# Kernel optimization log

Hardware: AMD Instinct MI355X
Metric: run time of the kernel (lower is better)

## Reference

```python
import jax, jax.numpy as jnp
import numpy as np
import math


def get_alibi_slopes(n_heads: int) -> np.ndarray:
    # Bloom-style ALiBi slopes.
    cp2 = 2 ** math.floor(math.log2(n_heads))
    base = 2.0 ** (-(2.0 ** -(math.log2(cp2) - 3)))
    slopes = base ** np.arange(1, cp2 + 1, dtype=np.float32)
    if cp2 != n_heads:
        extra_base = 2.0 ** (-(2.0 ** -(math.log2(2 * cp2) - 3)))
        extra = extra_base ** np.arange(1, 2 * (n_heads - cp2) + 1, 2, dtype=np.float32)
        slopes = np.concatenate([slopes, extra])
    return slopes.astype(np.float32)


def setup_inputs() -> dict:
    key = jax.random.key(0)
    k1, k2, k3 = jax.random.split(key, 3)
    B, S, D, H = 2, 2048, 2048, 16
    T = B * S
    return {
        "hidden_states": jax.random.normal(k1, (T, D), dtype=jnp.float32) * 0.02,
        "qkv_weight": jax.random.normal(k2, (3, D, D), dtype=jnp.float32) * 0.02,
        "o_proj_weight": jax.random.normal(k3, (D, D), dtype=jnp.float32) * 0.02,
        "batch": B,
        "seq_len": S,
        "n_heads": H,
    }


def reference(hidden_states, qkv_weight, o_proj_weight, batch, seq_len, n_heads):
    T, D = hidden_states.shape
    head_dim = D // n_heads
    sm_scale = 1.0 / math.sqrt(head_dim)
    slopes = jnp.asarray(get_alibi_slopes(n_heads))  # [H]

    # QKV projection: equivalent of bmm(hidden.expand(3,-1,-1), qkv_weight)
    qkv = jnp.einsum("td,cde->cte", hidden_states, qkv_weight)  # [3, T, D]
    q, k, v = qkv.reshape(3, batch, seq_len, n_heads, head_dim)

    # Varlen causal attention with ALiBi (prefill / context phase).
    scores = jnp.einsum("bqhd,bkhd->bhqk", q, k) * sm_scale  # [B,H,S,S]
    pos = jnp.arange(seq_len)
    rel = (pos[None, :] - pos[:, None]).astype(jnp.float32)  # k_idx - q_idx
    scores = scores + slopes[None, :, None, None] * rel[None, None]
    causal = pos[None, :] <= pos[:, None]  # [S,S]
    scores = jnp.where(causal[None, None], scores, jnp.finfo(scores.dtype).min)
    probs = jax.nn.softmax(scores, axis=-1)
    attn = jnp.einsum("bhqk,bkhd->bqhd", probs, v)  # [B,S,H,Dh]

    attn = attn.reshape(T, D)
    return attn @ o_proj_weight
```

## Files before the change

### kernel.cpp

```cpp
#include <hip/hip_runtime.h>
#include <math.h>
#include <stdint.h>

typedef __bf16 bf16x8_t __attribute__((ext_vector_type(8)));
typedef float  f32x4_t  __attribute__((ext_vector_type(4)));
typedef unsigned short u16;


__device__ __forceinline__ u16 f2bf(float f) {
  unsigned u = __float_as_uint(f);
  u += 0x7FFFu + ((u >> 16) & 1u);
  return (u16)(u >> 16);
}

__device__ __forceinline__ u16 bf16bits(float f) {
  __bf16 b = (__bf16)f;
  return __builtin_bit_cast(u16, b);
}

__device__ __forceinline__ void gload_lds16(const u16* gsrc, u16* ldst) {
  __builtin_amdgcn_global_load_lds(
      (__attribute__((address_space(1))) void*)(const_cast<u16*>(gsrc)),
      (__attribute__((address_space(3))) void*)(ldst),
      16, 0, 0);
}

__device__ __forceinline__ int sw8(int row, int e) { return e ^ ((row & 7) << 3); }

__device__ __forceinline__ void store_out(float* C, long idx, float v) { C[idx] = v; }
__device__ __forceinline__ void store_out(u16* C, long idx, float v) { C[idx] = f2bf(v); }

__device__ __forceinline__ float alibi_slope(int h, int H) {
  int cp2 = 1, lg = 0;
  while (cp2 * 2 <= H) { cp2 *= 2; lg++; }
  if (h < cp2) {
    double e = exp2((double)-(lg - 3));
    return (float)exp2(-e * (double)(h + 1));
  } else {
    double e = exp2((double)-(lg + 1 - 3));
    return (float)exp2(-e * (double)(2 * (h - cp2) + 1));
  }
}

#define FENCE() asm volatile("" ::: "memory")
#define BARRIER() do { FENCE(); __builtin_amdgcn_s_barrier(); \
                       __builtin_amdgcn_sched_barrier(0); FENCE(); } while (0)
#define WAITLGKM() do { asm volatile("s_waitcnt lgkmcnt(0)" ::: "memory"); \
                        __builtin_amdgcn_sched_barrier(0); } while (0)


__global__ __launch_bounds__(256) void k_cast_bf16(const float* __restrict__ in,
                                                   u16* __restrict__ out, long n) {
  long i = ((long)blockIdx.x * 256 + threadIdx.x) * 4;
  if (i + 3 < n) {
    float4 v = *reinterpret_cast<const float4*>(in + i);
    ushort4 o;
    o.x = f2bf(v.x); o.y = f2bf(v.y); o.z = f2bf(v.z); o.w = f2bf(v.w);
    *reinterpret_cast<ushort4*>(out + i) = o;
  }
}


__global__ __launch_bounds__(256) void k_transpose_cast4(const float* __restrict__ in0,
                                                         const float* __restrict__ in1,
                                                         u16* __restrict__ out,
                                                         int R, int C) {
  __shared__ float tile[32][33];
  const float* inz = (blockIdx.z < 3) ? (in0 + (long)blockIdx.z * R * C) : in1;
  u16* outz = out + (long)blockIdx.z * R * C;
  const int tx = threadIdx.x & 31, ty = threadIdx.x >> 5;
  const int r0 = blockIdx.y * 32, c0 = blockIdx.x * 32;
#pragma unroll
  for (int i = 0; i < 4; ++i)
    tile[ty + i * 8][tx] = inz[(long)(r0 + ty + i * 8) * C + c0 + tx];
  __syncthreads();
#pragma unroll
  for (int i = 0; i < 4; ++i)
    outz[(long)(c0 + ty + i * 8) * R + r0 + tx] = f2bf(tile[tx][ty + i * 8]);
}


__device__ __forceinline__ void stage16(const u16* __restrict__ g, long grow0, int K,
                                        int kt, int lr0, u16 (*lds)[64], int lane) {
  const int e = (lane & 7) * 8;
#pragma unroll
  for (int i = 0; i < 2; ++i) {
    const int r = lr0 + i * 8 + (lane >> 3);
    gload_lds16(g + (grow0 + r) * (long)K + kt + (e ^ ((r & 7) << 3)), &lds[lr0 + i * 8][0]);
  }
}

__device__ __forceinline__ void stage8(const u16* __restrict__ g, long grow0, int K,
                                       int kt, int lr0, u16 (*lds)[64], int lane) {
  const int e = (lane & 7) * 8;
  const int r = lr0 + (lane >> 3);
  gload_lds16(g + (grow0 + r) * (long)K + kt + (e ^ ((r & 7) << 3)), &lds[lr0][0]);
}


template <typename OUT_T>
__global__ __launch_bounds__(512, 2) void k_gemm8(const u16* __restrict__ A,
                                                  const u16* __restrict__ Bt,
                                                  OUT_T* __restrict__ Cb,
                                                  int M, int N, int K, long matStride,
                                                  float qs, u16* __restrict__ Vt) {
  __shared__ u16 As[2][256][64];
  __shared__ u16 Bs[2][256][64];

  const int tid = threadIdx.x, wid = tid >> 6, lane = tid & 63;
  const int wr = wid >> 2, wc = wid & 3;
  const int frow = lane & 15, fk8 = (lane >> 4) * 8;
  const int orow = (lane >> 4) * 4, ocol = lane & 15;

  const int nwg = gridDim.x * gridDim.y;
  const int orig = blockIdx.y * gridDim.x + blockIdx.x;
  const int q = nwg >> 3, rr = nwg & 7;
  const int xcd = orig & 7, sl = orig >> 3;
  const int wg = (xcd < rr ? xcd * (q + 1) : rr * (q + 1) + (xcd - rr) * q) + sl;
  const int by = wg / gridDim.x, bx = wg % gridDim.x;

  const long abase = (long)by * 256, bbase = (long)bx * 256;

  const int bg0 = (wid >> 1) * 64 + (wid & 1) * 16;
  const int ag0 = (wid >> 2) * 128 + (wid & 3) * 16;

  f32x4_t acc[8][4];
#pragma unroll
  for (int m = 0; m < 8; ++m)
#pragma unroll
    for (int n = 0; n < 4; ++n)
#pragma unroll
      for (int r = 0; r < 4; ++r) acc[m][n][r] = 0.f;

  const int nt = K >> 6;

  stage16(A, abase, K, 0, ag0, As[0], lane);
  stage16(Bt, bbase, K, 0, bg0, Bs[0], lane);
  stage16(Bt, bbase, K, 0, bg0 + 32, Bs[0], lane);
  stage16(A, abase, K, 0, ag0 + 64, As[0], lane);
  asm volatile("s_waitcnt vmcnt(4)" ::: "memory");
  BARRIER();

  bf16x8_t afr[4][2], bfr[4][2];
  int cur = 0;

  for (int t = 0; t < nt; ++t) {
    const int ktn = (t + 1) << 6;
    const bool hn = (t + 1 < nt);
    const int nb = cur ^ 1;

#pragma unroll
    for (int m = 0; m < 4; ++m) {
      const int r = wr * 128 + m * 16 + frow;
      afr[m][0] = *reinterpret_cast<const bf16x8_t*>(&As[cur][r][sw8(r, fk8)]);
      afr[m][1] = *reinterpret_cast<const bf16x8_t*>(&As[cur][r][sw8(r, 32 + fk8)]);
    }
#pragma unroll
    for (int n = 0; n < 2; ++n) {
      const int r = wc * 64 + n * 16 + frow;
      bfr[n][0] = *reinterpret_cast<const bf16x8_t*>(&Bs[cur][r][sw8(r, fk8)]);
      bfr[n][1] = *reinterpret_cast<const bf16x8_t*>(&Bs[cur][r][sw8(r, 32 + fk8)]);
    }
    if (hn) stage16(A, abase, K, ktn, ag0, As[nb], lane);
    BARRIER();
    WAITLGKM();
    __builtin_amdgcn_s_setprio(1);
#pragma unroll
    for (int m = 0; m < 4; ++m)
#pragma unroll
      for (int n = 0; n < 2; ++n) {
        acc[m][n] = __builtin_amdgcn_mfma_f32_16x16x32_bf16(afr[m][0], bfr[n][0], acc[m][n], 0, 0, 0);
        acc[m][n] = __builtin_amdgcn_mfma_f32_16x16x32_bf16(afr[m][1], bfr[n][1], acc[m][n], 0, 0, 0);
      }
    __builtin_amdgcn_s_setprio(0);
    if (hn) asm volatile("s_waitcnt vmcnt(4)" ::: "memory");
    else    asm volatile("s_waitcnt vmcnt(2)" ::: "memory");
    BARRIER();

#pragma unroll
    for (int n = 0; n < 2; ++n) {
      const int r = wc * 64 + 32 + n * 16 + frow;
      bfr[2 + n][0] = *reinterpret_cast<const bf16x8_t*>(&Bs[cur][r][sw8(r, fk8)]);
      bfr[2 + n][1] = *reinterpret_cast<const bf16x8_t*>(&Bs[cur][r][sw8(r, 32 + fk8)]);
    }
    if (hn) stage16(Bt, bbase, K, ktn, bg0, Bs[nb], lane);
    BARRIER();
    WAITLGKM();
    __builtin_amdgcn_s_setprio(1);
#pragma unroll
    for (int m = 0; m < 4; ++m)
#pragma unroll
      for (int n = 0; n < 2; ++n) {
        acc[m][2 + n] = __builtin_amdgcn_mfma_f32_16x16x32_bf16(afr[m][0], bfr[2 + n][0], acc[m][2 + n], 0, 0, 0);
        acc[m][2 + n] = __builtin_amdgcn_mfma_f32_16x16x32_bf16(afr[m][1], bfr[2 + n][1], acc[m][2 + n], 0, 0, 0);
      }
    __builtin_amdgcn_s_setprio(0);
    if (!hn) asm volatile("s_waitcnt vmcnt(0)" ::: "memory");
    BARRIER();

#pragma unroll
    for (int m = 0; m < 4; ++m) {
      const int r = wr * 128 + 64 + m * 16 + frow;
      afr[m][0] = *reinterpret_cast<const bf16x8_t*>(&As[cur][r][sw8(r, fk8)]);
      afr[m][1] = *reinterpret_cast<const bf16x8_t*>(&As[cur][r][sw8(r, 32 + fk8)]);
    }
    if (hn) stage16(Bt, bbase, K, ktn, bg0 + 32, Bs[nb], lane);
    BARRIER();
    WAITLGKM();
    __builtin_amdgcn_s_setprio(1);
#pragma unroll
    for (int m = 0; m < 4; ++m)
#pragma unroll
      for (int n = 0; n < 2; ++n) {
        acc[4 + m][n] = __builtin_amdgcn_mfma_f32_16x16x32_bf16(afr[m][0], bfr[n][0], acc[4 + m][n], 0, 0, 0);
        acc[4 + m][n] = __builtin_amdgcn_mfma_f32_16x16x32_bf16(afr[m][1], bfr[n][1], acc[4 + m][n], 0, 0, 0);
      }
    __builtin_amdgcn_s_setprio(0);
    BARRIER();

    if (hn) stage16(A, abase, K, ktn, ag0 + 64, As[nb], lane);
    __builtin_amdgcn_s_setprio(1);
#pragma unroll
    for (int m = 0; m < 4; ++m)
#pragma unroll
      for (int n = 0; n < 2; ++n) {
        acc[4 + m][2 + n] = __builtin_amdgcn_mfma_f32_16x16x32_bf16(afr[m][0], bfr[2 + n][0], acc[4 + m][2 + n], 0, 0, 0);
        acc[4 + m][2 + n] = __builtin_amdgcn_mfma_f32_16x16x32_bf16(afr[m][1], bfr[2 + n][1], acc[4 + m][2 + n], 0, 0, 0);
      }
    __builtin_amdgcn_s_setprio(0);
    if (hn) asm volatile("s_waitcnt vmcnt(4)" ::: "memory");
    BARRIER();

    cur ^= 1;
  }

  const int mat = (int)(bbase >> 11);
  if (Vt != nullptr && mat == 2) {
#pragma unroll
    for (int m = 0; m < 8; ++m)
#pragma unroll
      for (int n = 0; n < 4; ++n)
#pragma unroll
        for (int r = 0; r < 4; ++r) {
          const long row = abase + wr * 128 + m * 16 + orow + r;
          const int col = (int)bbase + wc * 64 + n * 16 + ocol;
          const int e = col & 2047, hh = e >> 7, dd = e & 127;
          const long bb = row >> 11, ss = row & 2047;
          Vt[(((bb << 4) + hh) * 128 + dd) * 2048 + ss] = bf16bits(acc[m][n][r]);
        }
  } else {
#pragma unroll
    for (int m = 0; m < 8; ++m)
#pragma unroll
      for (int n = 0; n < 4; ++n)
#pragma unroll
        for (int r = 0; r < 4; ++r) {
          const long row = abase + wr * 128 + m * 16 + orow + r;
          const int col = (int)bbase + wc * 64 + n * 16 + ocol;
          const float sc = (mat == 0) ? qs : 1.0f;
          const long idx = (long)mat * matStride + row * 2048 + (col & 2047);
          store_out(Cb, idx, acc[m][n][r] * sc);
        }
  }
}


template <typename OUT_T>
__global__ __launch_bounds__(512, 2) void k_gemm2(const u16* __restrict__ A,
                                                  const u16* __restrict__ Bt,
                                                  OUT_T* __restrict__ Cb,
                                                  int M, int N, int K, long matStride,
                                                  float qs) {
  __shared__ u16 As[2][128][64];
  __shared__ u16 Bs[2][256][64];

  const int tid = threadIdx.x, wid = tid >> 6, lane = tid & 63;
  const int wr = wid >> 2, wc = wid & 3;
  const int frow = lane & 15, fk8 = (lane >> 4) * 8;
  const int orow = (lane >> 4) * 4, ocol = lane & 15;

  const int nwg = gridDim.x * gridDim.y;
  const int orig = blockIdx.y * gridDim.x + blockIdx.x;
  const int q = nwg >> 3, rr = nwg & 7;
  const int xcd = orig & 7, sl = orig >> 3;
  const int wg = (xcd < rr ? xcd * (q + 1) : rr * (q + 1) + (xcd - rr) * q) + sl;
  const int by = wg / gridDim.x, bx = wg % gridDim.x;

  const long abase = (long)by * 128, bbase = (long)bx * 256;

  const int bg0 = (wid >> 1) * 64 + (wid & 1) * 16;
  const int ag0 = ((wid & 1) << 6) + ((wid >> 1) << 3);

  f32x4_t acc[4][4];
#pragma unroll
  for (int m = 0; m < 4; ++m)
#pragma unroll
    for (int n = 0; n < 4; ++n)
#pragma unroll
      for (int r = 0; r < 4; ++r) acc[m][n][r] = 0.f;

  const int nt = K >> 6;

  stage16(Bt, bbase, K, 0, bg0, Bs[0], lane);
  stage16(Bt, bbase, K, 0, bg0 + 32, Bs[0], lane);
  stage8 (A,  abase, K, 0, ag0, As[0], lane);
  stage8 (A,  abase, K, 0, ag0 + 32, As[0], lane);
  asm volatile("s_waitcnt vmcnt(1)" ::: "memory");
  BARRIER();

  bf16x8_t bfr[4][2], afr[2][2];
  int cur = 0;

  for (int t = 0; t < nt; ++t) {
    const int ktn = (t + 1) << 6;
    const bool hn = (t + 1 < nt);
    const int nb = cur ^ 1;

#pragma unroll
    for (int n = 0; n < 4; ++n) {
      const int r = wc * 64 + n * 16 + frow;
      bfr[n][0] = *reinterpret_cast<const bf16x8_t*>(&Bs[cur][r][sw8(r, fk8)]);
      bfr[n][1] = *reinterpret_cast<const bf16x8_t*>(&Bs[cur][r][sw8(r, 32 + fk8)]);
    }
#pragma unroll
    for (int m = 0; m < 2; ++m) {
      const int r = wr * 64 + m * 16 + frow;
      afr[m][0] = *reinterpret_cast<const bf16x8_t*>(&As[cur][r][sw8(r, fk8)]);
      afr[m][1] = *reinterpret_cast<const bf16x8_t*>(&As[cur][r][sw8(r, 32 + fk8)]);
    }
    if (hn) {
      stage16(Bt, bbase, K, ktn, bg0, Bs[nb], lane);
      stage16(Bt, bbase, K, ktn, bg0 + 32, Bs[nb], lane);
    }
    BARRIER();
    WAITLGKM();
    __builtin_amdgcn_s_setprio(1);
#pragma unroll
    for (int m = 0; m < 2; ++m)
#pragma unroll
      for (int n = 0; n < 4; ++n) {
        acc[m][n] = __builtin_amdgcn_mfma_f32_16x16x32_bf16(afr[m][0], bfr[n][0], acc[m][n], 0, 0, 0);
        acc[m][n] = __builtin_amdgcn_mfma_f32_16x16x32_bf16(afr[m][1], bfr[n][1], acc[m][n], 0, 0, 0);
      }
    __builtin_amdgcn_s_setprio(0);
    if (hn) asm volatile("s_waitcnt vmcnt(4)" ::: "memory");
    else    asm volatile("s_waitcnt vmcnt(0)" ::: "memory");
    BARRIER();

#pragma unroll
    for (int m = 0; m < 2; ++m) {
      const int r = wr * 64 + 32 + m * 16 + frow;
      afr[m][0] = *reinterpret_cast<const bf16x8_t*>(&As[cur][r][sw8(r, fk8)]);
      afr[m][1] = *reinterpret_cast<const bf16x8_t*>(&As[cur][r][sw8(r, 32 + fk8)]);
    }
    if (hn) {
      stage8(A, abase, K, ktn, ag0, As[nb], lane);
      stage8(A, abase, K, ktn, ag0 + 32, As[nb], lane);
    }
    BARRIER();
    WAITLGKM();
    __builtin_amdgcn_s_setprio(1);
#pragma unroll
    for (int m = 0; m < 2; ++m)
#pragma unroll
      for (int n = 0; n < 4; ++n) {
        acc[2 + m][n] = __builtin_amdgcn_mfma_f32_16x16x32_bf16(afr[m][0], bfr[n][0], acc[2 + m][n], 0, 0, 0);
        acc[2 + m][n] = __builtin_amdgcn_mfma_f32_16x16x32_bf16(afr[m][1], bfr[n][1], acc[2 + m][n], 0, 0, 0);
      }
    __builtin_amdgcn_s_setprio(0);
    if (hn) asm volatile("s_waitcnt vmcnt(1)" ::: "memory");
    BARRIER();

    cur ^= 1;
  }

#pragma unroll
  for (int m = 0; m < 4; ++m)
#pragma unroll
    for (int n = 0; n < 4; ++n)
#pragma unroll
      for (int r = 0; r < 4; ++r) {
        const long row = abase + wr * 64 + m * 16 + orow + r;
        const int col = (int)bbase + wc * 64 + n * 16 + ocol;
        const float sc = ((col >> 11) == 0) ? qs : 1.0f;
        const long idx = (long)(col >> 11) * matStride + row * 2048 + (col & 2047);
        store_out(Cb, idx, acc[m][n][r] * sc);
      }
}


__global__ __launch_bounds__(256) void k_attn(const u16* __restrict__ Q,
                                              const u16* __restrict__ Kb,
                                              const u16* __restrict__ Vt,
                                              u16* __restrict__ Out,
                                              int B, int S, int H, int D,
                                              float log2e) {
  __shared__ u16 Ks[2][64][128];
  __shared__ u16 Vs[2][128][64];
  __shared__ u16 Ps[64][64];

  const int tid = threadIdx.x, wid = tid >> 6, lane = tid & 63;

  const int nq = gridDim.x, nbh = gridDim.y;
  const int lin = blockIdx.x + nq * blockIdx.y;
  const int qb0 = lin / nbh;
  const int bh  = lin % nbh;
  const int qb  = (qb0 < nq / 2) ? qb0 : (nq + nq / 2 - 1 - qb0);

  const int b = bh / H, h = bh % H;
  const int Dh = D / H;

  const float slope2 = alibi_slope(h, H) * log2e;
  const long qrow0 = (long)b * S + qb * 64 + wid * 16;

  const int frow = lane & 15;
  const int fk8  = (lane >> 4) * 8;
  const int orow = (lane >> 4) * 4;
  const int ocol = lane & 15;

  bf16x8_t aq[4];
#pragma unroll
  for (int kk = 0; kk < 4; ++kk)
    aq[kk] = *reinterpret_cast<const bf16x8_t*>(
        Q + (qrow0 + frow) * (long)D + h * Dh + kk * 32 + fk8);

  float cw[4];
#pragma unroll
  for (int n = 0; n < 4; ++n) cw[n] = slope2 * (float)(n * 16 + ocol);

  f32x4_t oacc[8];
#pragma unroll
  for (int no = 0; no < 8; ++no)
#pragma unroll
    for (int r = 0; r < 4; ++r) oacc[no][r] = 0.f;

  float Mrun[4], lrun[4];
#pragma unroll
  for (int r = 0; r < 4; ++r) { Mrun[r] = -3.0e38f; lrun[r] = 0.f; }

  const u16* kbase = Kb + (long)b * S * D + h * Dh;
  const u16* vbase = Vt + (long)bh * Dh * S;

  auto STAGE = [&](int kt, int bi) {
#pragma unroll
    for (int i = 0; i < 4; ++i) {
      const int lr = i * 16 + wid * 4;
      const int r  = lr + (lane >> 4);
      gload_lds16(kbase + ((long)kt * 64 + r) * (long)D + sw8(r, (lane & 15) * 8),
                  &Ks[bi][lr][0]);
    }
#pragma unroll
    for (int i = 0; i < 4; ++i) {
      const int lr = i * 32 + wid * 8;
      const int r  = lr + (lane >> 3);
      gload_lds16(vbase + (long)r * S + kt * 64 + sw8(r, (lane & 7) * 8),
                  &Vs[bi][lr][0]);
    }
  };

  STAGE(qb, 0);
  asm volatile("s_waitcnt vmcnt(0)" ::: "memory");
  BARRIER();

  int cur = 0;

  for (int kt = qb; kt >= 0; --kt) {
    if (kt > 0) STAGE(kt - 1, cur ^ 1);

    f32x4_t sacc[4];
#pragma unroll
    for (int n = 0; n < 4; ++n)
#pragma unroll
      for (int r = 0; r < 4; ++r) sacc[n][r] = 0.f;

    __builtin_amdgcn_s_setprio(1);
#pragma unroll
    for (int kk = 0; kk < 4; ++kk) {
      bf16x8_t bk[4];
#pragma unroll
      for (int n = 0; n < 4; ++n) {
        const int krow = n * 16 + frow;
        bk[n] = *reinterpret_cast<const bf16x8_t*>(&Ks[cur][krow][sw8(krow, kk * 32 + fk8)]);
      }
#pragma unroll
      for (int n = 0; n < 4; ++n)
        sacc[n] = __builtin_amdgcn_mfma_f32_16x16x32_bf16(aq[kk], bk[n], sacc[n], 0, 0, 0);
    }
    __builtin_amdgcn_s_setprio(0);

    const float tb = slope2 * (float)(kt << 6);
    float cbn[4];
#pragma unroll
    for (int n = 0; n < 4; ++n) cbn[n] = tb + cw[n];

    float tmax[4];
#pragma unroll
    for (int r = 0; r < 4; ++r) tmax[r] = -3.0e38f;

    if (kt == qb) {
#pragma unroll
      for (int n = 0; n < 4; ++n)
#pragma unroll
        for (int r = 0; r < 4; ++r) {
          float v = sacc[n][r] + cbn[n];
          v = (n * 16 + ocol <= wid * 16 + orow + r) ? v : -1.0e30f;
          sacc[n][r] = v;
          tmax[r] = fmaxf(tmax[r], v);
        }
    } else {
#pragma unroll
      for (int n = 0; n < 4; ++n)
#pragma unroll
        for (int r = 0; r < 4; ++r) {
          const float v = sacc[n][r] + cbn[n];
          sacc[n][r] = v;
          tmax[r] = fmaxf(tmax[r], v);
        }
    }
#pragma unroll
    for (int r = 0; r < 4; ++r) {
      float t = tmax[r];
      t = fmaxf(t, __shfl_xor(t, 1));
      t = fmaxf(t, __shfl_xor(t, 2));
      t = fmaxf(t, __shfl_xor(t, 4));
      t = fmaxf(t, __shfl_xor(t, 8));
      tmax[r] = t;
    }

    int need = 0;
#pragma unroll
    for (int r = 0; r < 4; ++r) need |= (tmax[r] > Mrun[r] + 11.0f) ? 1 : 0;
    if (__any(need)) {
#pragma unroll
      for (int r = 0; r < 4; ++r) {
        const float mnew = fmaxf(Mrun[r], tmax[r]);
        const float alpha = exp2f(Mrun[r] - mnew);
        Mrun[r] = mnew;
        lrun[r] *= alpha;
#pragma unroll
        for (int no = 0; no < 8; ++no) oacc[no][r] *= alpha;
      }
    }

    float tsum[4];
#pragma unroll
    for (int r = 0; r < 4; ++r) tsum[r] = 0.f;
#pragma unroll
    for (int n = 0; n < 4; ++n)
#pragma unroll
      for (int r = 0; r < 4; ++r) {
        const float p = exp2f(sacc[n][r] - Mrun[r]);
        tsum[r] += p;
        const int prow = wid * 16 + orow + r;
        Ps[prow][sw8(prow, n * 16 + ocol)] = bf16bits(p);
      }
#pragma unroll
    for (int r = 0; r < 4; ++r) {
      float t = tsum[r];
      t += __shfl_xor(t, 1);
      t += __shfl_xor(t, 2);
      t += __shfl_xor(t, 4);
      t += __shfl_xor(t, 8);
      lrun[r] += t;
    }

    WAITLGKM();
    BARRIER();

    __builtin_amdgcn_s_setprio(1);
#pragma unroll
    for (int kk = 0; kk < 2; ++kk) {
      const int prow = wid * 16 + frow;
      bf16x8_t pa = *reinterpret_cast<const bf16x8_t*>(&Ps[prow][sw8(prow, kk * 32 + fk8)]);
#pragma unroll
      for (int no = 0; no < 8; ++no) {
        const int vrow = no * 16 + frow;
        bf16x8_t bv = *reinterpret_cast<const bf16x8_t*>(&Vs[cur][vrow][sw8(vrow, kk * 32 + fk8)]);
        oacc[no] = __builtin_amdgcn_mfma_f32_16x16x32_bf16(pa, bv, oacc[no], 0, 0, 0);
      }
    }
    __builtin_amdgcn_s_setprio(0);

    if (kt > 0) {
      asm volatile("s_waitcnt vmcnt(0)" ::: "memory");
      BARRIER();
      cur ^= 1;
    }
  }

#pragma unroll
  for (int r = 0; r < 4; ++r) {
    const float rl = 1.0f / lrun[r];
    const long trow = qrow0 + orow + r;
#pragma unroll
    for (int no = 0; no < 8; ++no)
      Out[trow * (long)D + h * Dh + no * 16 + ocol] = bf16bits(oacc[no][r] * rl);
  }
}


extern "C" void kernel_launch(void* const* d_in, const int* in_sizes, int n_in,
                              void* d_out, int out_size, void* d_ws, size_t ws_size,
                              hipStream_t stream) {
  const float* hs   = (const float*)d_in[0];
  const float* qkvw = (const float*)d_in[1];
  const float* ow   = (const float*)d_in[2];

  const int D = 2048, B = 2, H = 16;
  const long TD = (long)in_sizes[0];
  const long DD = (long)in_sizes[2];
  const int T = (int)(TD / D);
  const int S = T / B;
  const int Dh = D / H;
  const float log2e = 1.44269504f;
  const float qs = (1.0f / sqrtf((float)Dh)) * log2e;

  u16* ws  = (u16*)d_ws;
  u16* hsb = ws;
  u16* wt  = ws + TD;
  u16* owt = wt + 3 * DD;
  u16* qkv = owt + DD;
  u16* vt   = qkv + 2 * TD;
  u16* attn = hsb;

  k_cast_bf16<<<dim3((unsigned)(TD / 1024)), 256, 0, stream>>>(hs, hsb, TD);
  k_transpose_cast4<<<dim3(D / 32, D / 32, 4), 256, 0, stream>>>(qkvw, ow, wt, D, D);
  k_gemm8<u16><<<dim3((3 * D) / 256, T / 256), 512, 0, stream>>>(
      hsb, wt, qkv, T, 3 * D, D, TD, qs, vt);
  k_attn<<<dim3(S / 64, B * H), 256, 0, stream>>>(
      qkv, qkv + TD, vt, attn, B, S, H, D, log2e);
  k_gemm2<float><<<dim3(D / 256, T / 128), 512, 0, stream>>>(
      attn, owt, (float*)d_out, T, D, D, 0L, 1.0f);
}
```

Before: 283.4 us.

## Enlarge attention query tile to 128 rows with two M-subtiles per wave

Each attention block now handles 128 query rows instead of 64, and each wave computes two 16-row subtiles against the same K and V tiles in shared memory. This halves the number of K/V tile loads per query row and doubles the MFMA work per LDS read of K/V. Waves whose rows lie entirely before the current key tile skip compute but still join the barriers. In exchange the grid is halved, register pressure rises from the doubled accumulators, and causal work is less balanced across waves.

```diff
diff --git a/kernel.cpp b/kernel.cpp
--- a/kernel.cpp
+++ b/kernel.cpp
@@ -397,7 +397,7 @@
                                               float log2e) {
   __shared__ u16 Ks[2][64][128];
   __shared__ u16 Vs[2][128][64];
-  __shared__ u16 Ps[64][64];
+  __shared__ u16 Ps[128][64];
 
   const int tid = threadIdx.x, wid = tid >> 6, lane = tid & 63;
 
@@ -411,32 +411,39 @@
   const int Dh = D / H;
 
   const float slope2 = alibi_slope(h, H) * log2e;
-  const long qrow0 = (long)b * S + qb * 64 + wid * 16;
+  const long qrow0 = (long)b * S + qb * 128 + wid * 32;
+  const int qg0 = qb * 128 + wid * 32;
 
   const int frow = lane & 15;
   const int fk8  = (lane >> 4) * 8;
   const int orow = (lane >> 4) * 4;
   const int ocol = lane & 15;
 
-  bf16x8_t aq[4];
-#pragma unroll
-  for (int kk = 0; kk < 4; ++kk)
-    aq[kk] = *reinterpret_cast<const bf16x8_t*>(
-        Q + (qrow0 + frow) * (long)D + h * Dh + kk * 32 + fk8);
+  bf16x8_t aq[2][4];
+#pragma unroll
+  for (int m = 0; m < 2; ++m)
+#pragma unroll
+    for (int kk = 0; kk < 4; ++kk)
+      aq[m][kk] = *reinterpret_cast<const bf16x8_t*>(
+          Q + (qrow0 + m * 16 + frow) * (long)D + h * Dh + kk * 32 + fk8);
 
   float cw[4];
 #pragma unroll
   for (int n = 0; n < 4; ++n) cw[n] = slope2 * (float)(n * 16 + ocol);
 
-  f32x4_t oacc[8];
-#pragma unroll
-  for (int no = 0; no < 8; ++no)
-#pragma unroll
-    for (int r = 0; r < 4; ++r) oacc[no][r] = 0.f;
-
-  float Mrun[4], lrun[4];
-#pragma unroll
-  for (int r = 0; r < 4; ++r) { Mrun[r] = -3.0e38f; lrun[r] = 0.f; }
+  f32x4_t oacc[2][8];
+#pragma unroll
+  for (int m = 0; m < 2; ++m)
+#pragma unroll
+    for (int no = 0; no < 8; ++no)
+#pragma unroll
+      for (int r = 0; r < 4; ++r) oacc[m][no][r] = 0.f;
+
+  float Mrun[2][4], lrun[2][4];
+#pragma unroll
+  for (int m = 0; m < 2; ++m)
+#pragma unroll
+    for (int r = 0; r < 4; ++r) { Mrun[m][r] = -3.0e38f; lrun[m][r] = 0.f; }
 
   const u16* kbase = Kb + (long)b * S * D + h * Dh;
   const u16* vbase = Vt + (long)bh * Dh * S;
@@ -458,128 +465,162 @@
     }
   };
 
-  STAGE(qb, 0);
+  STAGE(2 * qb + 1, 0);
   asm volatile("s_waitcnt vmcnt(0)" ::: "memory");
   BARRIER();
 
   int cur = 0;
 
-  for (int kt = qb; kt >= 0; --kt) {
+  for (int kt = 2 * qb + 1; kt >= 0; --kt) {
     if (kt > 0) STAGE(kt - 1, cur ^ 1);
 
-    f32x4_t sacc[4];
-#pragma unroll
-    for (int n = 0; n < 4; ++n)
-#pragma unroll
-      for (int r = 0; r < 4; ++r) sacc[n][r] = 0.f;
-
-    __builtin_amdgcn_s_setprio(1);
-#pragma unroll
-    for (int kk = 0; kk < 4; ++kk) {
-      bf16x8_t bk[4];
-#pragma unroll
-      for (int n = 0; n < 4; ++n) {
-        const int krow = n * 16 + frow;
-        bk[n] = *reinterpret_cast<const bf16x8_t*>(&Ks[cur][krow][sw8(krow, kk * 32 + fk8)]);
-      }
-#pragma unroll
-      for (int n = 0; n < 4; ++n)
-        sacc[n] = __builtin_amdgcn_mfma_f32_16x16x32_bf16(aq[kk], bk[n], sacc[n], 0, 0, 0);
-    }
-    __builtin_amdgcn_s_setprio(0);
-
-    const float tb = slope2 * (float)(kt << 6);
-    float cbn[4];
-#pragma unroll
-    for (int n = 0; n < 4; ++n) cbn[n] = tb + cw[n];
-
-    float tmax[4];
-#pragma unroll
-    for (int r = 0; r < 4; ++r) tmax[r] = -3.0e38f;
-
-    if (kt == qb) {
-#pragma unroll
-      for (int n = 0; n < 4; ++n)
+    const bool active = (kt * 64) <= (qg0 + 31);
+
+    if (active) {
+      f32x4_t sacc[2][4];
+#pragma unroll
+      for (int m = 0; m < 2; ++m)
+#pragma unroll
+        for (int n = 0; n < 4; ++n)
+#pragma unroll
+          for (int r = 0; r < 4; ++r) sacc[m][n][r] = 0.f;
+
+      __builtin_amdgcn_s_setprio(1);
+#pragma unroll
+      for (int kk = 0; kk < 4; ++kk) {
+        bf16x8_t bk[4];
+#pragma unroll
+        for (int n = 0; n < 4; ++n) {
+          const int krow = n * 16 + frow;
+          bk[n] = *reinterpret_cast<const bf16x8_t*>(&Ks[cur][krow][sw8(krow, kk * 32 + fk8)]);
+        }
+#pragma unroll
+        for (int m = 0; m < 2; ++m)
+#pragma unroll
+          for (int n = 0; n < 4; ++n)
+            sacc[m][n] = __builtin_amdgcn_mfma_f32_16x16x32_bf16(aq[m][kk], bk[n], sacc[m][n], 0, 0, 0);
+      }
+      __builtin_amdgcn_s_setprio(0);
+
+      const float tb = slope2 * (float)(kt << 6);
+      float cbn[4];
+#pragma unroll
+      for (int n = 0; n < 4; ++n) cbn[n] = tb + cw[n];
+
+      float tmax[2][4];
+#pragma unroll
+      for (int m = 0; m < 2; ++m)
+#pragma unroll
+        for (int r = 0; r < 4; ++r) tmax[m][r] = -3.0e38f;
+
+      if (kt >= 2 * qb) {
+#pragma unroll
+        for (int m = 0; m < 2; ++m)
+#pragma unroll
+          for (int n = 0; n < 4; ++n)
+#pragma unroll
+            for (int r = 0; r < 4; ++r) {
+              const int kg = (kt << 6) + n * 16 + ocol;
+              const int qg = qg0 + m * 16 + orow + r;
+              float v = sacc[m][n][r] + cbn[n];
+              v = (kg <= qg) ? v : -1.0e30f;
+              sacc[m][n][r] = v;
+              tmax[m][r] = fmaxf(tmax[m][r], v);
+            }
+      } else {
+#pragma unroll
+        for (int m = 0; m < 2; ++m)
+#pragma unroll
+          for (int n = 0; n < 4; ++n)
+#pragma unroll
+            for (int r = 0; r < 4; ++r) {
+              const float v = sacc[m][n][r] + cbn[n];
+              sacc[m][n][r] = v;
+              tmax[m][r] = fmaxf(tmax[m][r], v);
+            }
+      }
+#pragma unroll
+      for (int m = 0; m < 2; ++m)
 #pragma unroll
         for (int r = 0; r < 4; ++r) {
-          float v = sacc[n][r] + cbn[n];
-          v = (n * 16 + ocol <= wid * 16 + orow + r) ? v : -1.0e30f;
-          sacc[n][r] = v;
-          tmax[r] = fmaxf(tmax[r], v);
+          float t = tmax[m][r];
+          t = fmaxf(t, __shfl_xor(t, 1));
+          t = fmaxf(t, __shfl_xor(t, 2));
+          t = fmaxf(t, __shfl_xor(t, 4));
+          t = fmaxf(t, __shfl_xor(t, 8));
+          tmax[m][r] = t;
         }
-    } else {
-#pragma unroll
-      for (int n = 0; n < 4; ++n)
+
+      int need = 0;
+#pragma unroll
+      for (int m = 0; m < 2; ++m)
+#pragma unroll
+        for (int r = 0; r < 4; ++r) need |= (tmax[m][r] > Mrun[m][r] + 11.0f) ? 1 : 0;
+      if (__any(need)) {
+#pragma unroll
+        for (int m = 0; m < 2; ++m)
+#pragma unroll
+          for (int r = 0; r < 4; ++r) {
+            const float mnew = fmaxf(Mrun[m][r], tmax[m][r]);
+            const float alpha = exp2f(Mrun[m][r] - mnew);
+            Mrun[m][r] = mnew;
+            lrun[m][r] *= alpha;
+#pragma unroll
+            for (int no = 0; no < 8; ++no) oacc[m][no][r] *= alpha;
+          }
+      }
+
+      float tsum[2][4];
+#pragma unroll
+      for (int m = 0; m < 2; ++m)
+#pragma unroll
+        for (int r = 0; r < 4; ++r) tsum[m][r] = 0.f;
+#pragma unroll
+      for (int m = 0; m < 2; ++m)
+#pragma unroll
+        for (int n = 0; n < 4; ++n)
+#pragma unroll
+          for (int r = 0; r < 4; ++r) {
+            const float p = exp2f(sacc[m][n][r] - Mrun[m][r]);
+            tsum[m][r] += p;
+            const int prow = wid * 32 + m * 16 + orow + r;
+            Ps[prow][sw8(prow, n * 16 + ocol)] = bf16bits(p);
+          }
+#pragma unroll
+      for (int m = 0; m < 2; ++m)
 #pragma unroll
         for (int r = 0; r < 4; ++r) {
-          const float v = sacc[n][r] + cbn[n];
-          sacc[n][r] = v;
-          tmax[r] = fmaxf(tmax[r], v);
+          float t = tsum[m][r];
+          t += __shfl_xor(t, 1);
+          t += __shfl_xor(t, 2);
+          t += __shfl_xor(t, 4);
+          t += __shfl_xor(t, 8);
+          lrun[m][r] += t;
         }
     }
-#pragma unroll
-    for (int r = 0; r < 4; ++r) {
-      float t = tmax[r];
-      t = fmaxf(t, __shfl_xor(t, 1));
-      t = fmaxf(t, __shfl_xor(t, 2));
-      t = fmaxf(t, __shfl_xor(t, 4));
-      t = fmaxf(t, __shfl_xor(t, 8));
-      tmax[r] = t;
-    }
-
-    int need = 0;
-#pragma unroll
-    for (int r = 0; r < 4; ++r) need |= (tmax[r] > Mrun[r] + 11.0f) ? 1 : 0;
-    if (__any(need)) {
-#pragma unroll
-      for (int r = 0; r < 4; ++r) {
-        const float mnew = fmaxf(Mrun[r], tmax[r]);
-        const float alpha = exp2f(Mrun[r] - mnew);
-        Mrun[r] = mnew;
-        lrun[r] *= alpha;
-#pragma unroll
-        for (int no = 0; no < 8; ++no) oacc[no][r] *= alpha;
-      }
-    }
-
-    float tsum[4];
-#pragma unroll
-    for (int r = 0; r < 4; ++r) tsum[r] = 0.f;
-#pragma unroll
-    for (int n = 0; n < 4; ++n)
-#pragma unroll
-      for (int r = 0; r < 4; ++r) {
-        const float p = exp2f(sacc[n][r] - Mrun[r]);
-        tsum[r] += p;
-        const int prow = wid * 16 + orow + r;
-        Ps[prow][sw8(prow, n * 16 + ocol)] = bf16bits(p);
-      }
-#pragma unroll
-    for (int r = 0; r < 4; ++r) {
-      float t = tsum[r];
-      t += __shfl_xor(t, 1);
-      t += __shfl_xor(t, 2);
-      t += __shfl_xor(t, 4);
-      t += __shfl_xor(t, 8);
-      lrun[r] += t;
-    }
 
     WAITLGKM();
     BARRIER();
 
-    __builtin_amdgcn_s_setprio(1);
-#pragma unroll
-    for (int kk = 0; kk < 2; ++kk) {
-      const int prow = wid * 16 + frow;
-      bf16x8_t pa = *reinterpret_cast<const bf16x8_t*>(&Ps[prow][sw8(prow, kk * 32 + fk8)]);
-#pragma unroll
-      for (int no = 0; no < 8; ++no) {
-        const int vrow = no * 16 + frow;
-        bf16x8_t bv = *reinterpret_cast<const bf16x8_t*>(&Vs[cur][vrow][sw8(vrow, kk * 32 + fk8)]);
-        oacc[no] = __builtin_amdgcn_mfma_f32_16x16x32_bf16(pa, bv, oacc[no], 0, 0, 0);
-      }
-    }
-    __builtin_amdgcn_s_setprio(0);
+    if (active) {
+      __builtin_amdgcn_s_setprio(1);
+#pragma unroll
+      for (int kk = 0; kk < 2; ++kk) {
+        bf16x8_t pa[2];
+        const int prow0 = wid * 32 + frow;
+        const int prow1 = wid * 32 + 16 + frow;
+        pa[0] = *reinterpret_cast<const bf16x8_t*>(&Ps[prow0][sw8(prow0, kk * 32 + fk8)]);
+        pa[1] = *reinterpret_cast<const bf16x8_t*>(&Ps[prow1][sw8(prow1, kk * 32 + fk8)]);
+#pragma unroll
+        for (int no = 0; no < 8; ++no) {
+          const int vrow = no * 16 + frow;
+          bf16x8_t bv = *reinterpret_cast<const bf16x8_t*>(&Vs[cur][vrow][sw8(vrow, kk * 32 + fk8)]);
+          oacc[0][no] = __builtin_amdgcn_mfma_f32_16x16x32_bf16(pa[0], bv, oacc[0][no], 0, 0, 0);
+          oacc[1][no] = __builtin_amdgcn_mfma_f32_16x16x32_bf16(pa[1], bv, oacc[1][no], 0, 0, 0);
+        }
+      }
+      __builtin_amdgcn_s_setprio(0);
+    }
 
     if (kt > 0) {
       asm volatile("s_waitcnt vmcnt(0)" ::: "memory");
@@ -589,13 +630,15 @@
   }
 
 #pragma unroll
-  for (int r = 0; r < 4; ++r) {
-    const float rl = 1.0f / lrun[r];
-    const long trow = qrow0 + orow + r;
-#pragma unroll
-    for (int no = 0; no < 8; ++no)
-      Out[trow * (long)D + h * Dh + no * 16 + ocol] = bf16bits(oacc[no][r] * rl);
-  }
+  for (int m = 0; m < 2; ++m)
+#pragma unroll
+    for (int r = 0; r < 4; ++r) {
+      const float rl = 1.0f / lrun[m][r];
+      const long trow = qrow0 + m * 16 + orow + r;
+#pragma unroll
+      for (int no = 0; no < 8; ++no)
+        Out[trow * (long)D + h * Dh + no * 16 + ocol] = bf16bits(oacc[m][no][r] * rl);
+    }
 }
 
 
@@ -627,7 +670,7 @@
   k_transpose_cast4<<<dim3(D / 32, D / 32, 4), 256, 0, stream>>>(qkvw, ow, wt, D, D);
   k_gemm8<u16><<<dim3((3 * D) / 256, T / 256), 512, 0, stream>>>(
       hsb, wt, qkv, T, 3 * D, D, TD, qs, vt);
-  k_attn<<<dim3(S / 64, B * H), 256, 0, stream>>>(
+  k_attn<<<dim3(S / 128, B * H), 256, 0, stream>>>(
       qkv, qkv + TD, vt, attn, B, S, H, D, log2e);
   k_gemm2<float><<<dim3(D / 256, T / 128), 512, 0, stream>>>(
       attn, owt, (float*)d_out, T, D, D, 0L, 1.0f);
```

Measured after the change: 313.1 us. 10.5% more time.
